# Kernel tuning notes

Hardware: AMD Instinct MI355X
Metric: run time of the kernel (lower is better)

## Reference

```python
import jax, jax.numpy as jnp
import numpy as np

B, C1, H, W = 8, 256, 192, 192
P = 4              # effective patch size (even, <= H,W)
ROUTE_RATIO = 0.25
MIN_REGIONS = 1
HIDDEN = 128       # max(int(c1*0.5), 16)
ROUTE_HIDDEN = 64  # max(HIDDEN//2, 16)
EPS = 1e-5


def conv2d(x, w, groups=1, pad=0):
    return jax.lax.conv_general_dilated(
        x, w, (1, 1), [(pad, pad), (pad, pad)],
        dimension_numbers=("NCHW", "OIHW", "NCHW"),
        feature_group_count=groups)


def bn(x, g, b):
    # eval-mode BatchNorm with running_mean=0, running_var=1
    scale = g / jnp.sqrt(1.0 + EPS)
    return x * scale[None, :, None, None] + b[None, :, None, None]


def pixel_unshuffle(x, r):
    n, c, h, w = x.shape
    x = x.reshape(n, c, h // r, r, w // r, r)
    return x.transpose(0, 1, 3, 5, 2, 4).reshape(n, c * r * r, h // r, w // r)


def pixel_shuffle(x, r):
    n, cr, h, w = x.shape
    c = cr // (r * r)
    x = x.reshape(n, c, r, r, h, w)
    return x.transpose(0, 1, 4, 2, 5, 3).reshape(n, c, h * r, w * r)


def setup_inputs() -> dict:
    key = jax.random.key(0)
    ks = jax.random.split(key, 8)
    c4 = C1 * 4
    inp = {
        "x": jax.random.normal(ks[0], (B, C1, H, W), jnp.float32),
        # route head: 1x1 conv (no bias) -> BN -> SiLU -> 1x1 conv (bias)
        "rw1": jax.random.normal(ks[1], (ROUTE_HIDDEN, C1, 1, 1), jnp.float32) / np.sqrt(C1),
        "rg1": jnp.ones((ROUTE_HIDDEN,), jnp.float32),
        "rb1": jnp.zeros((ROUTE_HIDDEN,), jnp.float32),
        "rw2": jax.random.normal(ks[2], (1, ROUTE_HIDDEN, 1, 1), jnp.float32) / np.sqrt(ROUTE_HIDDEN),
        "rbias2": jnp.zeros((1,), jnp.float32),
        # expert: Conv(4c->hidden,1x1)+BN+SiLU, DWConv(3x3)+BN+SiLU, Conv(hidden->4c,1x1)+BN
        "ew1": jax.random.normal(ks[3], (HIDDEN, c4, 1, 1), jnp.float32) / np.sqrt(c4),
        "eg1": jnp.ones((HIDDEN,), jnp.float32),
        "eb1": jnp.zeros((HIDDEN,), jnp.float32),
        "dww": jax.random.normal(ks[4], (HIDDEN, 1, 3, 3), jnp.float32) / 3.0,
        "dwg": jnp.ones((HIDDEN,), jnp.float32),
        "dwb": jnp.zeros((HIDDEN,), jnp.float32),
        "ew2": jax.random.normal(ks[5], (c4, HIDDEN, 1, 1), jnp.float32) / np.sqrt(HIDDEN),
        "eg2": jnp.ones((c4,), jnp.float32),
        "eb2": jnp.zeros((c4,), jnp.float32),
    }
    return inp


def reference(x, rw1, rg1, rb1, rw2, rbias2, ew1, eg1, eb1, dww, dwg, dwb, ew2, eg2, eb2):
    b, c, h, w = x.shape
    p = P
    pad_h = (p - h % p) % p
    pad_w = (p - w % p) % p
    x_pad = jnp.pad(x, ((0, 0), (0, 0), (0, pad_h), (0, pad_w)))
    hp, wp = h + pad_h, w + pad_w
    gh, gw = hp // p, wp // p
    num_patches = gh * gw
    k = min(num_patches, max(MIN_REGIONS, int(np.ceil(num_patches * ROUTE_RATIO))))

    # router: avg-pool each patch, 1x1 MLP -> per-patch score
    pooled = x_pad.reshape(b, c, gh, p, gw, p).mean(axis=(3, 5))          # [b,c,gh,gw]
    r1 = jax.nn.silu(bn(conv2d(pooled, rw1), rg1, rb1))
    logits = conv2d(r1, rw2) + rbias2[None, :, None, None]
    scores = jax.nn.sigmoid(logits).reshape(b, num_patches)               # [b,N]
    top_vals, top_idx = jax.lax.top_k(scores, k)                          # [b,k]

    # gather selected patches
    patches = x_pad.reshape(b, c, gh, p, gw, p).transpose(0, 2, 4, 1, 3, 5)
    patches = patches.reshape(b, num_patches, c, p, p)
    sel = jnp.take_along_axis(patches, top_idx[:, :, None, None, None], axis=1)
    sel = sel.reshape(b * k, c, p, p)

    # expert on pixel-unshuffled patches
    y = pixel_unshuffle(sel, 2)                                           # [bk, 4c, p/2, p/2]
    y = jax.nn.silu(bn(conv2d(y, ew1), eg1, eb1))
    y = jax.nn.silu(bn(conv2d(y, dww, groups=HIDDEN, pad=1), dwg, dwb))
    y = bn(conv2d(y, ew2), eg2, eb2)
    refined = pixel_shuffle(y, 2).reshape(b, k, c, p, p)
    refined = refined * top_vals[:, :, None, None, None]

    # scatter back into zero residual
    delta = jnp.zeros((b, num_patches, c, p, p), x.dtype)
    delta = delta.at[jnp.arange(b)[:, None], top_idx].set(refined)
    delta = delta.reshape(b, gh, gw, c, p, p).transpose(0, 3, 1, 4, 2, 5)
    delta = delta.reshape(b, c, hp, wp)
    return delta[..., :h, :w]
```

## Files before the change

### kernel.cpp

```cpp
#include <hip/hip_runtime.h>
#include <hip/hip_bf16.h>

typedef __attribute__((ext_vector_type(8))) short bf16x8;
typedef __attribute__((ext_vector_type(4))) float f32x4;

#define NB 8
#define C1 256
#define HH 192
#define WW 192
#define GH 48
#define GW 48
#define NP 2304
#define KSEL 576
#define RH 64
#define HID 128
#define C4 1024
#define HW (HH*WW)

#define WS_FLAG 0
#define WS_F 64
#define WS_W16 81280ull
#define WS_POOLED 605696ull
#define WS_PSCALE WS_POOLED
#define WS_SCORES 19480064ull

#define F_RW1 0
#define F_RG1 16384
#define F_RB1 16448
#define F_RW2 16512
#define F_RBIAS2 16576
#define F_EG1 16580
#define F_EB1 16708
#define F_DWW 16836
#define F_DWG 17988
#define F_DWB 18116
#define F_EG2 18244
#define F_EB2 19268

__device__ __forceinline__ float b2f(unsigned short h) {
  return __uint_as_float(((unsigned)h) << 16);
}
__device__ __forceinline__ unsigned short f2b(float f) {
  unsigned u = __float_as_uint(f);
  u += 0x7FFF + ((u >> 16) & 1u);
  return (unsigned short)(u >> 16);
}
__device__ __forceinline__ float siluf(float v) { return v / (1.f + expf(-v)); }

__global__ void k_detect(const unsigned short* xb, char* ws) {
  __shared__ int cnt[256];
  int t = threadIdx.x;
  int c = 0;
#pragma unroll
  for (int s = 0; s < 8; ++s) {
    unsigned short u = xb[(size_t)(t * 8 + s) * 1024];
    int e = (u >> 7) & 0xFF;
    c += (u == 0 || (e >= 90 && e <= 145)) ? 1 : 0;
  }
  cnt[t] = c;
  __syncthreads();
  for (int s = 128; s > 0; s >>= 1) {
    if (t < s) cnt[t] += cnt[t + s];
    __syncthreads();
  }
  if (t == 0) *(int*)(ws + WS_FLAG) = (cnt[0] >= 1229) ? 1 : 0;
}

__global__ void k_prep(const void* rw1, const void* rg1, const void* rb1, const void* rw2,
                       const void* rbias2, const void* ew1, const void* eg1, const void* eb1,
                       const void* dww, const void* dwg, const void* dwb, const void* ew2,
                       const void* eg2, const void* eb2, char* ws) {
  int bf = *(const int*)(ws + WS_FLAG);
  float* F = (float*)(ws + WS_F);
  unsigned short* W16 = (unsigned short*)(ws + WS_W16);
  int i = blockIdx.x * 256 + threadIdx.x;
  if (i >= 282433) return;
  if (i < 20289) {
    const void* src; int si; int dof;
    if      (i < 16384) { src = rw1;    si = i;          dof = F_RW1 + si; }
    else if (i < 16448) { src = rg1;    si = i - 16384;  dof = F_RG1 + si; }
    else if (i < 16512) { src = rb1;    si = i - 16448;  dof = F_RB1 + si; }
    else if (i < 16576) { src = rw2;    si = i - 16512;  dof = F_RW2 + si; }
    else if (i < 16577) { src = rbias2; si = i - 16576;  dof = F_RBIAS2 + si; }
    else if (i < 16705) { src = eg1;    si = i - 16577;  dof = F_EG1 + si; }
    else if (i < 16833) { src = eb1;    si = i - 16705;  dof = F_EB1 + si; }
    else if (i < 17985) { src = dww;    si = i - 16833;  dof = F_DWW + si; }
    else if (i < 18113) { src = dwg;    si = i - 17985;  dof = F_DWG + si; }
    else if (i < 18241) { src = dwb;    si = i - 18113;  dof = F_DWB + si; }
    else if (i < 19265) { src = eg2;    si = i - 18241;  dof = F_EG2 + si; }
    else                { src = eb2;    si = i - 19265;  dof = F_EB2 + si; }
    F[dof] = bf ? b2f(((const unsigned short*)src)[si]) : ((const float*)src)[si];
  } else {
    int j = i - 20289;
    const void* src; int si; int dof;
    if (j < 131072) { src = ew1; si = j;          dof = j; }
    else            { src = ew2; si = j - 131072; dof = j; }
    W16[dof] = bf ? ((const unsigned short*)src)[si]
                  : f2b(((const float*)src)[si]);
  }
}

__global__ void k_pool(const void* xin, char* ws) {
  const int bf = *(const int*)(ws + WS_FLAG);
  float* pooled = (float*)(ws + WS_POOLED);
  int tid = blockIdx.x * 256 + threadIdx.x;
  int px = tid % GW;
  int t2 = tid / GW;
  int py = t2 % GH;
  int bc = t2 / GH;
  size_t base = (size_t)bc * HW + (size_t)(py * 4) * WW + px * 4;
  float s = 0.f;
  if (bf) {
#pragma unroll
    for (int r = 0; r < 4; ++r) {
      const ushort4 v = *(const ushort4*)((const unsigned short*)xin + base + r * WW);
      s += b2f(v.x) + b2f(v.y) + b2f(v.z) + b2f(v.w);
    }
  } else {
#pragma unroll
    for (int r = 0; r < 4; ++r) {
      const float4 v = *(const float4*)((const float*)xin + base + r * WW);
      s += v.x + v.y + v.z + v.w;
    }
  }
  pooled[tid] = s * 0.0625f;
}

__global__ __launch_bounds__(512, 2) void k_mlp(char* ws) {
  const float* F = (const float*)(ws + WS_F);
  const float* pooled = (const float*)(ws + WS_POOLED);
  float* scores = (float*)(ws + WS_SCORES);
  __shared__ float LP[256][68];
  __shared__ float LR[8 * 64];
  const int t = threadIdx.x;
  const int b = blockIdx.x / 36;
  const int pos0 = (blockIdx.x % 36) * 64;

  {
    const int pc = t & 15, c0 = t >> 4;
    const float* src = pooled + (size_t)(b * C1) * NP + pos0 + pc * 4;
#pragma unroll
    for (int s = 0; s < 8; ++s) {
      int c = c0 + 32 * s;
      float4 v = *(const float4*)(src + (size_t)c * NP);
      *(float4*)&LP[c][pc * 4] = v;
    }
  }
  __syncthreads();

  const int lane = t & 63;
  const int q = __builtin_amdgcn_readfirstlane(t >> 6);
  const float* wq = F + F_RW1 + q * 8 * C1;
  float acc[8];
#pragma unroll
  for (int j = 0; j < 8; ++j) acc[j] = 0.f;
  for (int c = 0; c < 256; c += 4) {
    float p0 = LP[c + 0][lane];
    float p1 = LP[c + 1][lane];
    float p2 = LP[c + 2][lane];
    float p3 = LP[c + 3][lane];
#pragma unroll
    for (int j = 0; j < 8; ++j) {
      acc[j] += wq[j * C1 + c + 0] * p0;
      acc[j] += wq[j * C1 + c + 1] * p1;
      acc[j] += wq[j * C1 + c + 2] * p2;
      acc[j] += wq[j * C1 + c + 3] * p3;
    }
  }
  const float BNS = 1.f / sqrtf(1.f + 1e-5f);
  float lp = 0.f;
#pragma unroll
  for (int j = 0; j < 8; ++j) {
    int h = q * 8 + j;
    float v = acc[j] * (F[F_RG1 + h] * BNS) + F[F_RB1 + h];
    lp += F[F_RW2 + h] * siluf(v);
  }
  LR[q * 64 + lane] = lp;
  __syncthreads();
  if (t < 64) {
    float s = F[F_RBIAS2];
#pragma unroll
    for (int j = 0; j < 8; ++j) s += LR[j * 64 + t];
    scores[b * NP + pos0 + t] = 1.f / (1.f + expf(-s));
  }
}

__global__ void k_route(char* ws) {
  const float* scores = (const float*)(ws + WS_SCORES);
  float* pscale = (float*)(ws + WS_PSCALE);
  int b = blockIdx.x / 9, r = blockIdx.x % 9;
  __shared__ float s[NP];
  for (int i = threadIdx.x; i < NP; i += 256) s[i] = scores[b * NP + i];
  __syncthreads();
  int i = r * 256 + threadIdx.x;
  float si = s[i];
  int rank = 0;
  for (int j = 0; j < NP; ++j) {
    float sj = s[j];
    rank += (sj > si || (sj == si && j < i)) ? 1 : 0;
  }
  pscale[b * NP + i] = (rank < KSEL) ? si : 0.f;
}


#define XLOAD(P_, cc_) do { \
    if (sel) { \
      size_t o_ = (size_t)(cc_) * 16 * HW; \
      if (BF) { P_##h0 = *(const ushort4*)(xh + xoff0 + o_); \
                P_##h1 = *(const ushort4*)(xh + xoff1 + o_); } \
      else    { P_##f0 = *(const float4*)(xf + xoff0 + o_); \
                P_##f1 = *(const float4*)(xf + xoff1 + o_); } \
    } \
    const unsigned short* wp_ = W1b + (cc_) * 64; \
    P_##w0 = *(const uint4*)(wp_ + wi0); \
    P_##w1 = *(const uint4*)(wp_ + wi1); \
  } while(0)

#define XWRITE(P_, UT_, WC_) do { \
    unsigned lo0_, hi0_, lo1_, hi1_; \
    if (BF) { lo0_ = P_##h0.x | ((unsigned)P_##h0.y << 16); hi0_ = P_##h0.z | ((unsigned)P_##h0.w << 16); \
              lo1_ = P_##h1.x | ((unsigned)P_##h1.y << 16); hi1_ = P_##h1.z | ((unsigned)P_##h1.w << 16); } \
    else    { asm("v_cvt_pk_bf16_f32 %0, %1, %2" : "=v"(lo0_) : "v"(P_##f0.x), "v"(P_##f0.y)); \
              asm("v_cvt_pk_bf16_f32 %0, %1, %2" : "=v"(hi0_) : "v"(P_##f0.z), "v"(P_##f0.w)); \
              asm("v_cvt_pk_bf16_f32 %0, %1, %2" : "=v"(lo1_) : "v"(P_##f1.x), "v"(P_##f1.y)); \
              asm("v_cvt_pk_bf16_f32 %0, %1, %2" : "=v"(hi1_) : "v"(P_##f1.z), "v"(P_##f1.w)); } \
    *(unsigned*)&UT_[n_lo72 + kb0] = lo0_; \
    *(unsigned*)&UT_[n_hi72 + kb0] = hi0_; \
    *(unsigned*)&UT_[n_lo72 + kb1] = lo1_; \
    *(unsigned*)&UT_[n_hi72 + kb1] = hi1_; \
    *(uint4*)&WC_[wcw0] = P_##w0; \
    *(uint4*)&WC_[wcw1] = P_##w1; \
  } while(0)

#define MFMA1(WCO_, B_, ACC_) ACC_ = __builtin_amdgcn_mfma_f32_16x16x32_bf16(*(const bf16x8*)&WC_[wc_off + (WCO_)], B_, ACC_, 0, 0, 0)

#define G1_MFMA(UT_, WCp_) do { \
    const unsigned short* WC_ = WCp_; \
    bf16x8 b0_ = *(const bf16x8*)&UT_[ut_off]; \
    bf16x8 b1_ = *(const bf16x8*)&UT_[ut_off + 32]; \
    MFMA1(0, b0_, acc10);    MFMA1(1152, b0_, acc11); \
    MFMA1(2304, b0_, acc12); MFMA1(3456, b0_, acc13); \
    MFMA1(32, b1_, acc10);   MFMA1(1152+32, b1_, acc11); \
    MFMA1(2304+32, b1_, acc12); MFMA1(3456+32, b1_, acc13); \
  } while(0)

#define G1EPI(ACC_, mi_) do { \
    _Pragma("unroll") \
    for (int r_ = 0; r_ < 4; ++r_) { \
      int h_ = 64 * wm + 16 * (mi_) + l4 * 4 + r_; \
      O1[h_ * 68 + otc] = siluf(ACC_[r_] * (F[F_EG1 + h_] * BNS) + F[F_EB1 + h_]); \
    } \
  } while(0)

#define G2_STEP(P_, WCp_, mt_) do { \
    const unsigned short* WC_ = WCp_; \
    *(uint4*)&((unsigned short*)WCp_)[w2a] = P_##a; \
    *(uint4*)&((unsigned short*)WCp_)[w2b] = P_##b; \
    if ((mt_) < 14) { \
      const unsigned short* wp_ = W2b + (size_t)((mt_) + 2) * 8192; \
      P_##a = *(const uint4*)(wp_ + w2s); \
      P_##b = *(const uint4*)(wp_ + w2s + 64); \
    } \
    __syncthreads(); \
    f32x4 a20 = (f32x4){0.f, 0.f, 0.f, 0.f}; \
    f32x4 a21 = (f32x4){0.f, 0.f, 0.f, 0.f}; \
    a20 = __builtin_amdgcn_mfma_f32_16x16x32_bf16(*(const bf16x8*)&WC_[g2_off + 0],        bq0, a20, 0,0,0); \
    a21 = __builtin_amdgcn_mfma_f32_16x16x32_bf16(*(const bf16x8*)&WC_[g2_off + 2176],     bq0, a21, 0,0,0); \
    a20 = __builtin_amdgcn_mfma_f32_16x16x32_bf16(*(const bf16x8*)&WC_[g2_off + 32],       bq1, a20, 0,0,0); \
    a21 = __builtin_amdgcn_mfma_f32_16x16x32_bf16(*(const bf16x8*)&WC_[g2_off + 2176+32],  bq1, a21, 0,0,0); \
    a20 = __builtin_amdgcn_mfma_f32_16x16x32_bf16(*(const bf16x8*)&WC_[g2_off + 64],       bq2, a20, 0,0,0); \
    a21 = __builtin_amdgcn_mfma_f32_16x16x32_bf16(*(const bf16x8*)&WC_[g2_off + 2176+64],  bq2, a21, 0,0,0); \
    a20 = __builtin_amdgcn_mfma_f32_16x16x32_bf16(*(const bf16x8*)&WC_[g2_off + 96],       bq3, a20, 0,0,0); \
    a21 = __builtin_amdgcn_mfma_f32_16x16x32_bf16(*(const bf16x8*)&WC_[g2_off + 2176+96],  bq3, a21, 0,0,0); \
    _Pragma("unroll") \
    for (int r_ = 0; r_ < 4; ++r_) { \
      int ml0_ = 32 * wm + l4 * 4 + r_; \
      int m20_ = (mt_) * 64 + ml0_; \
      OT[ml0_ * 68 + otc] = a20[r_] * (F[F_EG2 + m20_] * BNS) + F[F_EB2 + m20_]; \
      OT[(ml0_ + 16) * 68 + otc] = a21[r_] * (F[F_EG2 + m20_ + 16] * BNS) + F[F_EB2 + m20_ + 16]; \
    } \
    __syncthreads(); \
    _Pragma("unroll") \
    for (int s_ = 0; s_ < 2; ++s_) { \
      int cl_ = o_cl + 8 * s_; \
      int ch_ = (mt_) * 16 + cl_; \
      size_t ob_ = ((size_t)(bC1 + ch_) * HH + r0 + o_rr) * WW + c0 + o_p * 4; \
      int rb_ = (4 * cl_ + 2 * (o_rr & 1)) * 68 + (o_rr >> 1) * 32 + o_p; \
      float ps_ = PSs[o_p]; \
      float e0_ = OT[rb_] * ps_; \
      float e1_ = OT[rb_ + 68] * ps_; \
      float e2_ = OT[rb_ + 16] * ps_; \
      float e3_ = OT[rb_ + 68 + 16] * ps_; \
      if (BF) { ushort4 o4_ = {f2b(e0_), f2b(e1_), f2b(e2_), f2b(e3_)}; \
                *(ushort4*)((unsigned short*)outv + ob_) = o4_; } \
      else    { float4 o4_ = {e0_, e1_, e2_, e3_}; \
                *(float4*)((float*)outv + ob_) = o4_; } \
    } \
    __syncthreads(); \
  } while(0)

__global__ __launch_bounds__(512, 4) void k_expert(const void* xin, void* outv, char* ws) {
  const int BF = *(const int*)(ws + WS_FLAG);
  const float* F = (const float*)(ws + WS_F);
  const unsigned short* W1b = (const unsigned short*)(ws + WS_W16);
  const unsigned short* W2b = W1b + 131072;
  const float* pscale = (const float*)(ws + WS_PSCALE);

  __shared__ __align__(16) char LB[70720];
  unsigned short* UT0  = (unsigned short*)(LB);
  unsigned short* UT1  = (unsigned short*)(LB + 9216);
  unsigned short* WC0  = (unsigned short*)(LB + 18432);
  unsigned short* WC1  = (unsigned short*)(LB + 36864);
  float*          O1   = (float*)(LB + 18432);
  unsigned short* Y2T  = (unsigned short*)(LB);
  float*          OT   = (float*)(LB + 18432);
  unsigned short* WC20 = (unsigned short*)(LB + 35840);
  unsigned short* WC21 = (unsigned short*)(LB + 53248);
  float*          PSs  = (float*)(LB + 70656);

  const int t = threadIdx.x;
  const int lane = t & 63;
  const int w = t >> 6;
  const int wm = w >> 2, wn = w & 3;
  const int l15 = lane & 15, l4 = lane >> 4;
  const int bid = blockIdx.x;
  const int xq = bid % 3;
  const int py = (bid / 3) % GH;
  const int b  = bid / (3 * GH);
  const int r0 = py * 4, c0 = xq * 64;
  const int bC1 = b * C1;
  const float BNS = 1.f / sqrtf(1.f + 1e-5f);

  if (t < 16) PSs[t] = pscale[b * NP + py * GW + xq * 16 + t];
  __syncthreads();
  const bool sel = PSs[t & 15] != 0.f;

  const int rr = (t >> 4) & 3, v4 = t & 15;
  const int n_lo72 = (32 * (rr >> 1) + v4) * 72;
  const int n_hi72 = n_lo72 + 16 * 72;
  const int kb0 = 4 * w + 2 * (rr & 1);
  const int kb1 = kb0 + 32;
  const size_t xoff0 = ((size_t)bC1 + w) * HW + (size_t)(r0 + rr) * WW + c0 + v4 * 4;
  const size_t xoff1 = xoff0 + (size_t)8 * HW;
  const int m_0 = t >> 3, k8_0 = t & 7;
  const int wi0 = m_0 * 1024 + k8_0 * 8;
  const int wi1 = (m_0 + 64) * 1024 + k8_0 * 8;
  const int wcw0 = m_0 * 72 + k8_0 * 8;
  const int wcw1 = (m_0 + 64) * 72 + k8_0 * 8;
  const int ut_off = (16 * wn + l15) * 72 + l4 * 8;
  const int wc_off = (64 * wm + l15) * 72 + l4 * 8;
  const int otc = 16 * wn + l15;
  const int w2a = (t >> 3) * 136 + (t & 7) * 8;
  const int w2b = w2a + 64;
  const int w2s = (t >> 3) * 128 + (t & 7) * 8;
  const int g2_off = (32 * wm + l15) * 136 + l4 * 8;
  const int o_p = t & 15, o_rr = (t >> 4) & 3, o_cl = t >> 6;

  const float* xf = (const float*)xin;
  const unsigned short* xh = (const unsigned short*)xin;

  float4 Af0 = {0,0,0,0}, Af1 = {0,0,0,0}, Bf0 = {0,0,0,0}, Bf1 = {0,0,0,0};
  ushort4 Ah0 = {0,0,0,0}, Ah1 = {0,0,0,0}, Bh0 = {0,0,0,0}, Bh1 = {0,0,0,0};
  uint4 Aw0, Aw1, Bw0, Bw1;
  uint4 A2a, A2b, B2a, B2b;

  f32x4 acc10 = (f32x4){0.f,0.f,0.f,0.f};
  f32x4 acc11 = (f32x4){0.f,0.f,0.f,0.f};
  f32x4 acc12 = (f32x4){0.f,0.f,0.f,0.f};
  f32x4 acc13 = (f32x4){0.f,0.f,0.f,0.f};

  XLOAD(A, 0);
  XLOAD(B, 1);
  for (int cc2 = 0; cc2 < 8; ++cc2) {
    int cc = cc2 * 2;
    XWRITE(A, UT0, WC0);
    if (cc2 < 7) XLOAD(A, cc + 2);
    __syncthreads();
    G1_MFMA(UT0, WC0);
    XWRITE(B, UT1, WC1);
    if (cc2 < 7) XLOAD(B, cc + 3);
    __syncthreads();
    G1_MFMA(UT1, WC1);
  }

  A2a = *(const uint4*)(W2b + w2s);
  A2b = *(const uint4*)(W2b + w2s + 64);
  B2a = *(const uint4*)(W2b + 8192 + w2s);
  B2b = *(const uint4*)(W2b + 8192 + w2s + 64);

  __syncthreads();
  G1EPI(acc10, 0);
  G1EPI(acc11, 1);
  G1EPI(acc12, 2);
  G1EPI(acc13, 3);
  __syncthreads();

  {
    const int p = t & 15, hh = t >> 4;
#pragma unroll
    for (int s = 0; s < 4; ++s) {
      int h = hh + 32 * s;
      float i0 = O1[h * 68 + p];
      float i1 = O1[h * 68 + 16 + p];
      float i2 = O1[h * 68 + 32 + p];
      float i3 = O1[h * 68 + 48 + p];
      const float* kw = F + F_DWW + h * 9;
      float sd = F[F_DWG + h] * BNS, bd = F[F_DWB + h];
      float o00 = kw[4] * i0 + kw[5] * i1 + kw[7] * i2 + kw[8] * i3;
      float o01 = kw[3] * i0 + kw[4] * i1 + kw[6] * i2 + kw[7] * i3;
      float o10 = kw[1] * i0 + kw[2] * i1 + kw[4] * i2 + kw[5] * i3;
      float o11 = kw[0] * i0 + kw[1] * i1 + kw[3] * i2 + kw[4] * i3;
      Y2T[(0 * 16 + p) * 136 + h] = f2b(siluf(o00 * sd + bd));
      Y2T[(1 * 16 + p) * 136 + h] = f2b(siluf(o01 * sd + bd));
      Y2T[(2 * 16 + p) * 136 + h] = f2b(siluf(o10 * sd + bd));
      Y2T[(3 * 16 + p) * 136 + h] = f2b(siluf(o11 * sd + bd));
    }
  }
  __syncthreads();

  const int ybase = (16 * wn + l15) * 136 + l4 * 8;
  bf16x8 bq0 = *(const bf16x8*)&Y2T[ybase];
  bf16x8 bq1 = *(const bf16x8*)&Y2T[ybase + 32];
  bf16x8 bq2 = *(const bf16x8*)&Y2T[ybase + 64];
  bf16x8 bq3 = *(const bf16x8*)&Y2T[ybase + 96];

  for (int mtt = 0; mtt < 16; mtt += 2) {
    G2_STEP(A2, WC20, mtt);
    G2_STEP(B2, WC21, mtt + 1);
  }
}

extern "C" void kernel_launch(void* const* d_in, const int* in_sizes, int n_in,
                              void* d_out, int out_size, void* d_ws, size_t ws_size,
                              hipStream_t stream) {
  char* ws = (char*)d_ws;
  const void* x = d_in[0];
  k_detect<<<1, 256, 0, stream>>>((const unsigned short*)x, ws);
  k_prep<<<1104, 256, 0, stream>>>(d_in[1], d_in[2], d_in[3], d_in[4], d_in[5], d_in[6],
                                   d_in[7], d_in[8], d_in[9], d_in[10], d_in[11], d_in[12],
                                   d_in[13], d_in[14], ws);
  k_pool<<<18432, 256, 0, stream>>>(x, ws);
  k_mlp<<<288, 512, 0, stream>>>(ws);
  k_route<<<72, 256, 0, stream>>>(ws);
  k_expert<<<1152, 512, 0, stream>>>(x, d_out, ws);
}
```

Before: 319.9 us.

## Load expert weights directly from global into MFMA operands, shrink LDS

After: 517.0 us. 1.62x slower.

```diff
diff --git a/kernel.cpp b/kernel.cpp
--- a/kernel.cpp
+++ b/kernel.cpp
@@ -3,6 +3,7 @@
 
 typedef __attribute__((ext_vector_type(8))) short bf16x8;
 typedef __attribute__((ext_vector_type(4))) float f32x4;
+typedef __attribute__((ext_vector_type(2))) unsigned u32x2;
 
 #define NB 8
 #define C1 256
@@ -44,6 +45,11 @@
   unsigned u = __float_as_uint(f);
   u += 0x7FFF + ((u >> 16) & 1u);
   return (unsigned short)(u >> 16);
+}
+__device__ __forceinline__ unsigned pkbf(float a, float b) {
+  unsigned r;
+  asm("v_cvt_pk_bf16_f32 %0, %1, %2" : "=v"(r) : "v"(a), "v"(b));
+  return r;
 }
 __device__ __forceinline__ float siluf(float v) { return v / (1.f + expf(-v)); }
 
@@ -135,7 +141,6 @@
   const int t = threadIdx.x;
   const int b = blockIdx.x / 36;
   const int pos0 = (blockIdx.x % 36) * 64;
-
   {
     const int pc = t & 15, c0 = t >> 4;
     const float* src = pooled + (size_t)(b * C1) * NP + pos0 + pc * 4;
@@ -147,7 +152,6 @@
     }
   }
   __syncthreads();
-
   const int lane = t & 63;
   const int q = __builtin_amdgcn_readfirstlane(t >> 6);
   const float* wq = F + F_RW1 + q * 8 * C1;
@@ -203,75 +207,74 @@
 }
 
 
+#define MM(A_, B_, C_) C_ = __builtin_amdgcn_mfma_f32_16x16x32_bf16(A_, B_, C_, 0, 0, 0)
+
 #define XLOAD(P_, cc_) do { \
     if (sel) { \
       size_t o_ = (size_t)(cc_) * 16 * HW; \
-      if (BF) { P_##h0 = *(const ushort4*)(xh + xoff0 + o_); \
-                P_##h1 = *(const ushort4*)(xh + xoff1 + o_); } \
+      if (BF) { *(ushort4*)&P_##f0 = *(const ushort4*)(xh + xoff0 + o_); \
+                *(ushort4*)&P_##f1 = *(const ushort4*)(xh + xoff1 + o_); } \
       else    { P_##f0 = *(const float4*)(xf + xoff0 + o_); \
                 P_##f1 = *(const float4*)(xf + xoff1 + o_); } \
     } \
-    const unsigned short* wp_ = W1b + (cc_) * 64; \
-    P_##w0 = *(const uint4*)(wp_ + wi0); \
-    P_##w1 = *(const uint4*)(wp_ + wi1); \
   } while(0)
 
-#define XWRITE(P_, UT_, WC_) do { \
+#define XWRITE(P_, UT_) do { \
     unsigned lo0_, hi0_, lo1_, hi1_; \
-    if (BF) { lo0_ = P_##h0.x | ((unsigned)P_##h0.y << 16); hi0_ = P_##h0.z | ((unsigned)P_##h0.w << 16); \
-              lo1_ = P_##h1.x | ((unsigned)P_##h1.y << 16); hi1_ = P_##h1.z | ((unsigned)P_##h1.w << 16); } \
-    else    { asm("v_cvt_pk_bf16_f32 %0, %1, %2" : "=v"(lo0_) : "v"(P_##f0.x), "v"(P_##f0.y)); \
-              asm("v_cvt_pk_bf16_f32 %0, %1, %2" : "=v"(hi0_) : "v"(P_##f0.z), "v"(P_##f0.w)); \
-              asm("v_cvt_pk_bf16_f32 %0, %1, %2" : "=v"(lo1_) : "v"(P_##f1.x), "v"(P_##f1.y)); \
-              asm("v_cvt_pk_bf16_f32 %0, %1, %2" : "=v"(hi1_) : "v"(P_##f1.z), "v"(P_##f1.w)); } \
+    if (BF) { \
+      ushort4 u0_ = *(ushort4*)&P_##f0, u1_ = *(ushort4*)&P_##f1; \
+      lo0_ = u0_.x | ((unsigned)u0_.y << 16); hi0_ = u0_.z | ((unsigned)u0_.w << 16); \
+      lo1_ = u1_.x | ((unsigned)u1_.y << 16); hi1_ = u1_.z | ((unsigned)u1_.w << 16); \
+    } else { \
+      lo0_ = pkbf(P_##f0.x, P_##f0.y); hi0_ = pkbf(P_##f0.z, P_##f0.w); \
+      lo1_ = pkbf(P_##f1.x, P_##f1.y); hi1_ = pkbf(P_##f1.z, P_##f1.w); \
+    } \
     *(unsigned*)&UT_[n_lo72 + kb0] = lo0_; \
     *(unsigned*)&UT_[n_hi72 + kb0] = hi0_; \
     *(unsigned*)&UT_[n_lo72 + kb1] = lo1_; \
     *(unsigned*)&UT_[n_hi72 + kb1] = hi1_; \
-    *(uint4*)&WC_[wcw0] = P_##w0; \
-    *(uint4*)&WC_[wcw1] = P_##w1; \
   } while(0)
 
-#define MFMA1(WCO_, B_, ACC_) ACC_ = __builtin_amdgcn_mfma_f32_16x16x32_bf16(*(const bf16x8*)&WC_[wc_off + (WCO_)], B_, ACC_, 0, 0, 0)
-
-#define G1_MFMA(UT_, WCp_) do { \
-    const unsigned short* WC_ = WCp_; \
+#define G1_MFMA(UT_, cc_) do { \
+    const unsigned short* wp_ = w1base + (cc_) * 64; \
     bf16x8 b0_ = *(const bf16x8*)&UT_[ut_off]; \
     bf16x8 b1_ = *(const bf16x8*)&UT_[ut_off + 32]; \
-    MFMA1(0, b0_, acc10);    MFMA1(1152, b0_, acc11); \
-    MFMA1(2304, b0_, acc12); MFMA1(3456, b0_, acc13); \
-    MFMA1(32, b1_, acc10);   MFMA1(1152+32, b1_, acc11); \
-    MFMA1(2304+32, b1_, acc12); MFMA1(3456+32, b1_, acc13); \
+    bf16x8 a0_ = *(const bf16x8*)(wp_); \
+    bf16x8 a1_ = *(const bf16x8*)(wp_ + 16384); \
+    bf16x8 a2_ = *(const bf16x8*)(wp_ + 32768); \
+    bf16x8 a3_ = *(const bf16x8*)(wp_ + 49152); \
+    MM(a0_, b0_, acc10); MM(a1_, b0_, acc11); MM(a2_, b0_, acc12); MM(a3_, b0_, acc13); \
+    a0_ = *(const bf16x8*)(wp_ + 32); \
+    a1_ = *(const bf16x8*)(wp_ + 16384 + 32); \
+    a2_ = *(const bf16x8*)(wp_ + 32768 + 32); \
+    a3_ = *(const bf16x8*)(wp_ + 49152 + 32); \
+    MM(a0_, b1_, acc10); MM(a1_, b1_, acc11); MM(a2_, b1_, acc12); MM(a3_, b1_, acc13); \
   } while(0)
 
 #define G1EPI(ACC_, mi_) do { \
-    _Pragma("unroll") \
-    for (int r_ = 0; r_ < 4; ++r_) { \
-      int h_ = 64 * wm + 16 * (mi_) + l4 * 4 + r_; \
-      O1[h_ * 68 + otc] = siluf(ACC_[r_] * (F[F_EG1 + h_] * BNS) + F[F_EB1 + h_]); \
-    } \
+    const int h0_ = 64 * wm + 16 * (mi_) + l4 * 4; \
+    float g0_ = F[F_EG1 + h0_] * BNS,     c0_ = F[F_EB1 + h0_]; \
+    float g1_ = F[F_EG1 + h0_ + 1] * BNS, c1_ = F[F_EB1 + h0_ + 1]; \
+    float g2_ = F[F_EG1 + h0_ + 2] * BNS, c2_ = F[F_EB1 + h0_ + 2]; \
+    float g3_ = F[F_EG1 + h0_ + 3] * BNS, c3_ = F[F_EB1 + h0_ + 3]; \
+    unsigned lo_ = pkbf(siluf(ACC_[0] * g0_ + c0_), siluf(ACC_[1] * g1_ + c1_)); \
+    unsigned hi_ = pkbf(siluf(ACC_[2] * g2_ + c2_), siluf(ACC_[3] * g3_ + c3_)); \
+    *(u32x2*)&O1b[(16 * wn + l15) * 136 + h0_] = (u32x2){lo_, hi_}; \
   } while(0)
 
-#define G2_STEP(P_, WCp_, mt_) do { \
-    const unsigned short* WC_ = WCp_; \
-    *(uint4*)&((unsigned short*)WCp_)[w2a] = P_##a; \
-    *(uint4*)&((unsigned short*)WCp_)[w2b] = P_##b; \
-    if ((mt_) < 14) { \
-      const unsigned short* wp_ = W2b + (size_t)((mt_) + 2) * 8192; \
-      P_##a = *(const uint4*)(wp_ + w2s); \
-      P_##b = *(const uint4*)(wp_ + w2s + 64); \
-    } \
-    __syncthreads(); \
+#define G2_STEP(mt_) do { \
+    const unsigned short* wp_ = W2b + (size_t)((mt_) * 64 + 32 * wm + l15) * 128 + l4 * 8; \
     f32x4 a20 = (f32x4){0.f, 0.f, 0.f, 0.f}; \
     f32x4 a21 = (f32x4){0.f, 0.f, 0.f, 0.f}; \
-    a20 = __builtin_amdgcn_mfma_f32_16x16x32_bf16(*(const bf16x8*)&WC_[g2_off + 0],        bq0, a20, 0,0,0); \
-    a21 = __builtin_amdgcn_mfma_f32_16x16x32_bf16(*(const bf16x8*)&WC_[g2_off + 2176],     bq0, a21, 0,0,0); \
-    a20 = __builtin_amdgcn_mfma_f32_16x16x32_bf16(*(const bf16x8*)&WC_[g2_off + 32],       bq1, a20, 0,0,0); \
-    a21 = __builtin_amdgcn_mfma_f32_16x16x32_bf16(*(const bf16x8*)&WC_[g2_off + 2176+32],  bq1, a21, 0,0,0); \
-    a20 = __builtin_amdgcn_mfma_f32_16x16x32_bf16(*(const bf16x8*)&WC_[g2_off + 64],       bq2, a20, 0,0,0); \
-    a21 = __builtin_amdgcn_mfma_f32_16x16x32_bf16(*(const bf16x8*)&WC_[g2_off + 2176+64],  bq2, a21, 0,0,0); \
-    a20 = __builtin_amdgcn_mfma_f32_16x16x32_bf16(*(const bf16x8*)&WC_[g2_off + 96],       bq3, a20, 0,0,0); \
-    a21 = __builtin_amdgcn_mfma_f32_16x16x32_bf16(*(const bf16x8*)&WC_[g2_off + 2176+96],  bq3, a21, 0,0,0); \
+    bf16x8 a0_, a1_; \
+    a0_ = *(const bf16x8*)(wp_);            a1_ = *(const bf16x8*)(wp_ + 2048); \
+    MM(a0_, bq0, a20); MM(a1_, bq0, a21); \
+    a0_ = *(const bf16x8*)(wp_ + 32);       a1_ = *(const bf16x8*)(wp_ + 2048 + 32); \
+    MM(a0_, bq1, a20); MM(a1_, bq1, a21); \
+    a0_ = *(const bf16x8*)(wp_ + 64);       a1_ = *(const bf16x8*)(wp_ + 2048 + 64); \
+    MM(a0_, bq2, a20); MM(a1_, bq2, a21); \
+    a0_ = *(const bf16x8*)(wp_ + 96);       a1_ = *(const bf16x8*)(wp_ + 2048 + 96); \
+    MM(a0_, bq3, a20); MM(a1_, bq3, a21); \
     _Pragma("unroll") \
     for (int r_ = 0; r_ < 4; ++r_) { \
       int ml0_ = 32 * wm + l4 * 4 + r_; \
@@ -286,11 +289,10 @@
       int ch_ = (mt_) * 16 + cl_; \
       size_t ob_ = ((size_t)(bC1 + ch_) * HH + r0 + o_rr) * WW + c0 + o_p * 4; \
       int rb_ = (4 * cl_ + 2 * (o_rr & 1)) * 68 + (o_rr >> 1) * 32 + o_p; \
-      float ps_ = PSs[o_p]; \
-      float e0_ = OT[rb_] * ps_; \
-      float e1_ = OT[rb_ + 68] * ps_; \
-      float e2_ = OT[rb_ + 16] * ps_; \
-      float e3_ = OT[rb_ + 68 + 16] * ps_; \
+      float e0_ = OT[rb_] * ps; \
+      float e1_ = OT[rb_ + 68] * ps; \
+      float e2_ = OT[rb_ + 16] * ps; \
+      float e3_ = OT[rb_ + 68 + 16] * ps; \
       if (BF) { ushort4 o4_ = {f2b(e0_), f2b(e1_), f2b(e2_), f2b(e3_)}; \
                 *(ushort4*)((unsigned short*)outv + ob_) = o4_; } \
       else    { float4 o4_ = {e0_, e1_, e2_, e3_}; \
@@ -299,24 +301,20 @@
     __syncthreads(); \
   } while(0)
 
-__global__ __launch_bounds__(512, 4) void k_expert(const void* xin, void* outv, char* ws) {
+__global__ __launch_bounds__(512, 6) void k_expert(const void* xin, void* outv, char* ws) {
   const int BF = *(const int*)(ws + WS_FLAG);
   const float* F = (const float*)(ws + WS_F);
   const unsigned short* W1b = (const unsigned short*)(ws + WS_W16);
   const unsigned short* W2b = W1b + 131072;
   const float* pscale = (const float*)(ws + WS_PSCALE);
 
-  __shared__ __align__(16) char LB[70720];
-  unsigned short* UT0  = (unsigned short*)(LB);
-  unsigned short* UT1  = (unsigned short*)(LB + 9216);
-  unsigned short* WC0  = (unsigned short*)(LB + 18432);
-  unsigned short* WC1  = (unsigned short*)(LB + 36864);
-  float*          O1   = (float*)(LB + 18432);
-  unsigned short* Y2T  = (unsigned short*)(LB);
-  float*          OT   = (float*)(LB + 18432);
-  unsigned short* WC20 = (unsigned short*)(LB + 35840);
-  unsigned short* WC21 = (unsigned short*)(LB + 53248);
-  float*          PSs  = (float*)(LB + 70656);
+  __shared__ __align__(16) char LB[34880];
+  unsigned short* UT0 = (unsigned short*)(LB);
+  unsigned short* UT1 = (unsigned short*)(LB + 9216);
+  unsigned short* O1b = (unsigned short*)(LB);
+  unsigned short* Y2T = (unsigned short*)(LB + 17408);
+  float*          OT  = (float*)(LB);
+  float*          PSs = (float*)(LB + 34816);
 
   const int t = threadIdx.x;
   const int lane = t & 63;
@@ -333,7 +331,8 @@
 
   if (t < 16) PSs[t] = pscale[b * NP + py * GW + xq * 16 + t];
   __syncthreads();
-  const bool sel = PSs[t & 15] != 0.f;
+  const float ps = PSs[t & 15];
+  const bool sel = ps != 0.f;
 
   const int rr = (t >> 4) & 3, v4 = t & 15;
   const int n_lo72 = (32 * (rr >> 1) + v4) * 72;
@@ -342,27 +341,15 @@
   const int kb1 = kb0 + 32;
   const size_t xoff0 = ((size_t)bC1 + w) * HW + (size_t)(r0 + rr) * WW + c0 + v4 * 4;
   const size_t xoff1 = xoff0 + (size_t)8 * HW;
-  const int m_0 = t >> 3, k8_0 = t & 7;
-  const int wi0 = m_0 * 1024 + k8_0 * 8;
-  const int wi1 = (m_0 + 64) * 1024 + k8_0 * 8;
-  const int wcw0 = m_0 * 72 + k8_0 * 8;
-  const int wcw1 = (m_0 + 64) * 72 + k8_0 * 8;
   const int ut_off = (16 * wn + l15) * 72 + l4 * 8;
-  const int wc_off = (64 * wm + l15) * 72 + l4 * 8;
+  const unsigned short* w1base = W1b + (size_t)(64 * wm + l15) * 1024 + l4 * 8;
   const int otc = 16 * wn + l15;
-  const int w2a = (t >> 3) * 136 + (t & 7) * 8;
-  const int w2b = w2a + 64;
-  const int w2s = (t >> 3) * 128 + (t & 7) * 8;
-  const int g2_off = (32 * wm + l15) * 136 + l4 * 8;
   const int o_p = t & 15, o_rr = (t >> 4) & 3, o_cl = t >> 6;
 
   const float* xf = (const float*)xin;
   const unsigned short* xh = (const unsigned short*)xin;
 
   float4 Af0 = {0,0,0,0}, Af1 = {0,0,0,0}, Bf0 = {0,0,0,0}, Bf1 = {0,0,0,0};
-  ushort4 Ah0 = {0,0,0,0}, Ah1 = {0,0,0,0}, Bh0 = {0,0,0,0}, Bh1 = {0,0,0,0};
-  uint4 Aw0, Aw1, Bw0, Bw1;
-  uint4 A2a, A2b, B2a, B2b;
 
   f32x4 acc10 = (f32x4){0.f,0.f,0.f,0.f};
   f32x4 acc11 = (f32x4){0.f,0.f,0.f,0.f};
@@ -373,20 +360,15 @@
   XLOAD(B, 1);
   for (int cc2 = 0; cc2 < 8; ++cc2) {
     int cc = cc2 * 2;
-    XWRITE(A, UT0, WC0);
+    XWRITE(A, UT0);
     if (cc2 < 7) XLOAD(A, cc + 2);
     __syncthreads();
-    G1_MFMA(UT0, WC0);
-    XWRITE(B, UT1, WC1);
+    G1_MFMA(UT0, cc);
+    XWRITE(B, UT1);
     if (cc2 < 7) XLOAD(B, cc + 3);
     __syncthreads();
-    G1_MFMA(UT1, WC1);
-  }
-
-  A2a = *(const uint4*)(W2b + w2s);
-  A2b = *(const uint4*)(W2b + w2s + 64);
-  B2a = *(const uint4*)(W2b + 8192 + w2s);
-  B2b = *(const uint4*)(W2b + 8192 + w2s + 64);
+    G1_MFMA(UT1, cc + 1);
+  }
 
   __syncthreads();
   G1EPI(acc10, 0);
@@ -396,24 +378,28 @@
   __syncthreads();
 
   {
-    const int p = t & 15, hh = t >> 4;
+    const int dh = t & 127;
+    const int dgrp = t >> 7;
+    const float* kw = F + F_DWW + dh * 9;
+    float k0 = kw[0], k1 = kw[1], k2 = kw[2], k3 = kw[3], k4 = kw[4];
+    float k5 = kw[5], k6 = kw[6], k7 = kw[7], k8 = kw[8];
+    float sd = F[F_DWG + dh] * BNS, bd = F[F_DWB + dh];
 #pragma unroll
     for (int s = 0; s < 4; ++s) {
-      int h = hh + 32 * s;
-      float i0 = O1[h * 68 + p];
-      float i1 = O1[h * 68 + 16 + p];
-      float i2 = O1[h * 68 + 32 + p];
-      float i3 = O1[h * 68 + 48 + p];
-      const float* kw = F + F_DWW + h * 9;
-      float sd = F[F_DWG + h] * BNS, bd = F[F_DWB + h];
-      float o00 = kw[4] * i0 + kw[5] * i1 + kw[7] * i2 + kw[8] * i3;
-      float o01 = kw[3] * i0 + kw[4] * i1 + kw[6] * i2 + kw[7] * i3;
-      float o10 = kw[1] * i0 + kw[2] * i1 + kw[4] * i2 + kw[5] * i3;
-      float o11 = kw[0] * i0 + kw[1] * i1 + kw[3] * i2 + kw[4] * i3;
-      Y2T[(0 * 16 + p) * 136 + h] = f2b(siluf(o00 * sd + bd));
-      Y2T[(1 * 16 + p) * 136 + h] = f2b(siluf(o01 * sd + bd));
-      Y2T[(2 * 16 + p) * 136 + h] = f2b(siluf(o10 * sd + bd));
-      Y2T[(3 * 16 + p) * 136 + h] = f2b(siluf(o11 * sd + bd));
+      int patch = dgrp * 4 + s;
+      int nb = patch * 136 + dh;
+      float i0 = b2f(O1b[nb]);
+      float i1 = b2f(O1b[nb + 2176]);
+      float i2 = b2f(O1b[nb + 4352]);
+      float i3 = b2f(O1b[nb + 6528]);
+      float o00 = k4 * i0 + k5 * i1 + k7 * i2 + k8 * i3;
+      float o01 = k3 * i0 + k4 * i1 + k6 * i2 + k7 * i3;
+      float o10 = k1 * i0 + k2 * i1 + k4 * i2 + k5 * i3;
+      float o11 = k0 * i0 + k1 * i1 + k3 * i2 + k4 * i3;
+      Y2T[nb] = f2b(siluf(o00 * sd + bd));
+      Y2T[nb + 2176] = f2b(siluf(o01 * sd + bd));
+      Y2T[nb + 4352] = f2b(siluf(o10 * sd + bd));
+      Y2T[nb + 6528] = f2b(siluf(o11 * sd + bd));
     }
   }
   __syncthreads();
@@ -424,9 +410,8 @@
   bf16x8 bq2 = *(const bf16x8*)&Y2T[ybase + 64];
   bf16x8 bq3 = *(const bf16x8*)&Y2T[ybase + 96];
 
-  for (int mtt = 0; mtt < 16; mtt += 2) {
-    G2_STEP(A2, WC20, mtt);
-    G2_STEP(B2, WC21, mtt + 1);
+  for (int mt = 0; mt < 16; ++mt) {
+    G2_STEP(mt);
   }
 }
 
```
